# Performance work log

Hardware: AMD Instinct MI355X
Metric: run time of the kernel (lower is better)

Reference implementation:

```python
import jax, jax.numpy as jnp
import numpy as np

D_MODEL = 1024
POOL = 2048
K = 16
D_FF = 4096
N_HEADS = 16
TEMP = 1.0
EPS = 1e-5


def _ln(x, g, b):
    mu = jnp.mean(x, axis=-1, keepdims=True)
    var = jnp.mean((x - mu) ** 2, axis=-1, keepdims=True)
    return (x - mu) * jax.lax.rsqrt(var + EPS) * g + b


def setup_inputs() -> dict:
    key = jax.random.key(0)
    ks = jax.random.split(key, 12)
    s = 0.02
    return {
        "x": jax.random.normal(ks[0], (4, 1024, D_MODEL), jnp.float32),
        "w_router": s * jax.random.normal(ks[1], (D_MODEL, POOL), jnp.float32),
        "b_router": jnp.zeros((POOL,), jnp.float32),
        "firing": s * jax.random.normal(ks[2], (POOL, D_FF), jnp.float32),
        "w_pool_out": s * jax.random.normal(ks[3], (D_FF, D_MODEL), jnp.float32),
        "b_pool_out": jnp.zeros((D_MODEL,), jnp.float32),
        "w_in": s * jax.random.normal(ks[4], (D_MODEL, 3 * D_MODEL), jnp.float32),
        "b_in": jnp.zeros((3 * D_MODEL,), jnp.float32),
        "w_attn_out": s * jax.random.normal(ks[5], (D_MODEL, D_MODEL), jnp.float32),
        "b_attn_out": jnp.zeros((D_MODEL,), jnp.float32),
        "g1": jnp.ones((D_MODEL,), jnp.float32),
        "beta1": jnp.zeros((D_MODEL,), jnp.float32),
        "g2": jnp.ones((D_MODEL,), jnp.float32),
        "beta2": jnp.zeros((D_MODEL,), jnp.float32),
    }


def reference(x, w_router, b_router, firing, w_pool_out, b_pool_out,
              w_in, b_in, w_attn_out, b_attn_out, g1, beta1, g2, beta2):
    B, S, D = x.shape
    Hd = D // N_HEADS
    # --- Context router: score every neuron, select top-k, softmax weights ---
    scores = x @ w_router + b_router                      # [B,S,P]
    top_vals, top_idx = jax.lax.top_k(scores, K)          # [B,S,K]
    weights = jax.nn.softmax(top_vals / TEMP, axis=-1)    # [B,S,K]
    # --- Neuron pool: gather firing patterns, weighted combine, GELU, project ---
    patterns = firing[top_idx]                            # [B,S,K,d_ff] gather
    combined = jnp.einsum('bsk,bskf->bsf', weights, patterns)  # [B,S,d_ff]
    neuron_out = jax.nn.gelu(combined, approximate=False) @ w_pool_out + b_pool_out  # [B,S,D]
    # --- Self-attention over neuron_out (dropout inactive at eval) ---
    qkv = neuron_out @ w_in + b_in                        # [B,S,3D]
    q, k, v = jnp.split(qkv, 3, axis=-1)
    q = q.reshape(B, S, N_HEADS, Hd).transpose(0, 2, 1, 3)
    k = k.reshape(B, S, N_HEADS, Hd).transpose(0, 2, 1, 3)
    v = v.reshape(B, S, N_HEADS, Hd).transpose(0, 2, 1, 3)
    logits = jnp.einsum('bhqd,bhkd->bhqk', q, k) / jnp.sqrt(jnp.float32(Hd))
    probs = jax.nn.softmax(logits, axis=-1)
    ctx = jnp.einsum('bhqk,bhkd->bhqd', probs, v)
    ctx = ctx.transpose(0, 2, 1, 3).reshape(B, S, D)
    attn_out = ctx @ w_attn_out + b_attn_out
    # --- Residuals + norms ---
    h = _ln(x + attn_out, g1, beta1)
    out = _ln(h + neuron_out, g2, beta2)
    return out
```

## Files before the change

### kernel.cpp

```cpp
#include <hip/hip_runtime.h>
#include <math.h>

typedef __attribute__((ext_vector_type(8))) __bf16 bf16x8;
typedef __attribute__((ext_vector_type(4))) __bf16 bf16x4;
typedef __attribute__((ext_vector_type(4))) float f32x4;

#define DEV static __device__ __forceinline__

DEV float b2f(unsigned short u){ union{unsigned i; float f;} c; c.i=((unsigned)u)<<16; return c.f; }
DEV unsigned short f2b(float f){
  union{float f; unsigned u;} c; c.f=f;
  unsigned r = 0x7FFFu + ((c.u>>16)&1u);
  return (unsigned short)((c.u + r)>>16);
}
DEV unsigned pack2(float a, float b){ return (unsigned)f2b(a) | ((unsigned)f2b(b)<<16); }
DEV float gelu_exact(float x){ return 0.5f*x*(1.f+erff(x*0.70710678118654752f)); }

typedef __attribute__((address_space(1))) void gas_void;
typedef __attribute__((address_space(3))) void las_void;
DEV void gload_lds16(const unsigned short* g, unsigned short* l){
  __builtin_amdgcn_global_load_lds((const gas_void*)g, (las_void*)l, 16, 0, 0);
}

template<int N> DEV void waitcnt_vm(){
  if constexpr(N==0)      asm volatile("s_waitcnt vmcnt(0)" ::: "memory");
  else if constexpr(N==2) asm volatile("s_waitcnt vmcnt(2)" ::: "memory");
  else if constexpr(N==3) asm volatile("s_waitcnt vmcnt(3)" ::: "memory");
  else if constexpr(N==4) asm volatile("s_waitcnt vmcnt(4)" ::: "memory");
  else if constexpr(N==6) asm volatile("s_waitcnt vmcnt(6)" ::: "memory");
  else if constexpr(N==8) asm volatile("s_waitcnt vmcnt(8)" ::: "memory");
  else                    asm volatile("s_waitcnt vmcnt(0)" ::: "memory");
}

__global__ __launch_bounds__(256) void k_cast_bf16(const float* __restrict__ in,
                                                   unsigned short* __restrict__ out, long n4)
{
  long i = (long)blockIdx.x*256 + threadIdx.x;
  if (i >= n4) return;
  float4 v = ((const float4*)in)[i];
  ushort4 o; o.x=f2b(v.x); o.y=f2b(v.y); o.z=f2b(v.z); o.w=f2b(v.w);
  ((ushort4*)out)[i] = o;
}

__global__ __launch_bounds__(256) void k_transpose_cast(const float* __restrict__ in,
                                                        unsigned short* __restrict__ out,
                                                        int R, int C)
{
  __shared__ float tile[32][33];
  const int tc = blockIdx.x*32, tr = blockIdx.y*32;
  {
    const int r = threadIdx.x>>3, c4 = (threadIdx.x&7)*4;
    float4 v = *(const float4*)&in[(long)(tr+r)*C + tc+c4];
    tile[r][c4+0]=v.x; tile[r][c4+1]=v.y; tile[r][c4+2]=v.z; tile[r][c4+3]=v.w;
  }
  __syncthreads();
  {
    const int c = threadIdx.x>>3, r4 = (threadIdx.x&7)*4;
    ushort4 o;
    o.x = f2b(tile[r4+0][c]); o.y = f2b(tile[r4+1][c]);
    o.z = f2b(tile[r4+2][c]); o.w = f2b(tile[r4+3][c]);
    *(ushort4*)&out[(long)(tc+c)*R + tr+r4] = o;
  }
}

template<int WR, int WC, int FM, int FN, int OMODE>
__global__ __launch_bounds__(WR*WC*64, 2) void k_gemm_bt(
  const unsigned short* __restrict__ A, long lda, long sAb,
  const unsigned short* __restrict__ Bt, long ldb, long sBb,
  float* __restrict__ Cf, unsigned short* __restrict__ Cb, long ldc, long sCb,
  const float* __restrict__ bias, int Kiters)
{
  constexpr int WAVES = WR*WC;
  constexpr int BM = WR*FM*16, BN = WC*FN*16;
  constexpr int AR16 = BM/16, TOT16 = (BM+BN)/16;
  constexpr int UNITS = TOT16/WAVES;
  static_assert(TOT16 % WAVES == 0, "stage units must split across waves");
  __shared__ __align__(16) unsigned short S[3][TOT16*512];
  const int tid = threadIdx.x;
  const int wave = tid>>6, lane = tid&63;
  const int wr = wave/WC, wc = wave%WC;
  const int l15 = lane&15, lhi = lane>>4;
  const int lrow = lane>>2;
  const int lcol = ((lane&3) ^ ((lrow>>1)&3))*8;

  const int gx = gridDim.x;
  const int nwg = gx*gridDim.y;
  const int id = blockIdx.y*gx + blockIdx.x;
  const int sid = (id&7)*(nwg>>3) + (id>>3);
  const long bm = (long)(sid / gx)*BM, bn = (long)(sid % gx)*BN;

  const unsigned short* Ab  = A  + (long)blockIdx.z*sAb + bm*lda;
  const unsigned short* Btb = Bt + (long)blockIdx.z*sBb + bn*ldb;

  f32x4 acc[FM][FN];
  #pragma unroll
  for (int i=0;i<FM;i++)
    #pragma unroll
    for (int j=0;j<FN;j++) acc[i][j] = (f32x4){0.f,0.f,0.f,0.f};

  auto STAGE = [&](int kt, int buf){
    const long k0 = (long)kt*32;
    #pragma unroll
    for (int u=0; u<UNITS; ++u) {
      const int t = wave + u*WAVES;
      const unsigned short* g;
      if (t < AR16) g = Ab  + (long)(t*16 + lrow)*lda + k0 + lcol;
      else          g = Btb + (long)((t-AR16)*16 + lrow)*ldb + k0 + lcol;
      gload_lds16(g, &S[buf][t*512]);
    }
  };
  auto COMPUTE = [&](int buf){
    const unsigned short* Sb = S[buf];
    bf16x8 bfr[FN];
    #pragma unroll
    for (int j=0;j<FN;j++) {
      const int r = wc*(FN*16) + j*16 + l15;
      bfr[j] = *(const bf16x8*)&Sb[BM*32 + r*32 + ((lhi ^ ((r>>1)&3))*8)];
    }
    #pragma unroll
    for (int i=0;i<FM;i++) {
      const int r = wr*(FM*16) + i*16 + l15;
      bf16x8 a = *(const bf16x8*)&Sb[r*32 + ((lhi ^ ((r>>1)&3))*8)];
      #pragma unroll
      for (int j=0;j<FN;j++)
        acc[i][j] = __builtin_amdgcn_mfma_f32_16x16x32_bf16(a, bfr[j], acc[i][j], 0,0,0);
    }
  };

  STAGE(0, 0);
  if (Kiters > 1) STAGE(1, 1);
  for (int kt=0; kt<Kiters; ++kt) {
    if (kt+1 < Kiters) waitcnt_vm<UNITS>();
    else               waitcnt_vm<0>();
    __builtin_amdgcn_s_barrier();
    __builtin_amdgcn_sched_barrier(0);
    COMPUTE(kt%3);
    if (kt+2 < Kiters) STAGE(kt+2, (kt+2)%3);
  }

  #pragma unroll
  for (int i=0;i<FM;i++) {
    #pragma unroll
    for (int j=0;j<FN;j++) {
      long col = bn + wc*(FN*16) + j*16 + l15;
      float bb = bias ? bias[col] : 0.f;
      #pragma unroll
      for (int q=0;q<4;q++) {
        long row = bm + wr*(FM*16) + i*16 + lhi*4 + q;
        float v = acc[i][j][q] + bb;
        long off = (long)blockIdx.z*sCb + row*ldc + col;
        if constexpr (OMODE==0 || OMODE==2) Cf[off] = v;
        if constexpr (OMODE==1 || OMODE==2) Cb[off] = f2b(v);
      }
    }
  }
}

__global__ __launch_bounds__(256) void k_combine_bias_bf16(
    const unsigned short* __restrict__ p, long sz, const float* __restrict__ bias,
    unsigned short* __restrict__ outb)
{
  const long t = blockIdx.x;
  const int tid = threadIdx.x;
  ushort4 a = ((const ushort4*)(p + t*1024))[tid];
  ushort4 b = ((const ushort4*)(p + sz + t*1024))[tid];
  float4 bi = ((const float4*)bias)[tid];
  ushort4 o;
  o.x = f2b(b2f(a.x)+b2f(b.x)+bi.x); o.y = f2b(b2f(a.y)+b2f(b.y)+bi.y);
  o.z = f2b(b2f(a.z)+b2f(b.z)+bi.z); o.w = f2b(b2f(a.w)+b2f(b.w)+bi.w);
  ((ushort4*)(outb + t*1024))[tid] = o;
}

__global__ __launch_bounds__(256) void k_topk_softmax(const unsigned short* __restrict__ scores,
                                                      int* __restrict__ topidx,
                                                      float* __restrict__ topw)
{
  const int tid = threadIdx.x, wave = tid>>6, lane = tid&63;
  const long t = blockIdx.x;
  const unsigned short* row = scores + t*2048;
  const int base = wave*512 + lane*8;
  unsigned k0,k1,k2,k3,k4,k5,k6,k7;
  {
    uint4 v4 = *(const uint4*)(row + base);
    unsigned short u[8] = {
      (unsigned short)(v4.x&0xFFFF),(unsigned short)(v4.x>>16),
      (unsigned short)(v4.y&0xFFFF),(unsigned short)(v4.y>>16),
      (unsigned short)(v4.z&0xFFFF),(unsigned short)(v4.z>>16),
      (unsigned short)(v4.w&0xFFFF),(unsigned short)(v4.w>>16) };
    unsigned kk[8];
    #pragma unroll
    for (int e=0;e<8;e++){
      unsigned m = (u[e]&0x8000u) ? (unsigned)(~u[e] & 0xFFFFu)
                                  : ((unsigned)u[e] | 0x8000u);
      kk[e] = (m<<16) | (unsigned)(2047 - (base+e));
    }
    k0=kk[0];k1=kk[1];k2=kk[2];k3=kk[3];k4=kk[4];k5=kk[5];k6=kk[6];k7=kk[7];
  }
  #define CX(x,y) { unsigned mx = x>y?x:y, mn = x>y?y:x; x=mx; y=mn; }
  CX(k0,k1) CX(k2,k3) CX(k4,k5) CX(k6,k7)
  CX(k0,k2) CX(k1,k3) CX(k4,k6) CX(k5,k7)
  CX(k1,k2) CX(k5,k6)
  CX(k0,k4) CX(k1,k5) CX(k2,k6) CX(k3,k7)
  CX(k2,k4) CX(k3,k5)
  CX(k1,k2) CX(k3,k4) CX(k5,k6)
  #undef CX

  __shared__ unsigned wk[4][16];
  unsigned my1 = 0;
  for (int it=0; it<16; ++it){
    unsigned best = k0;
    #pragma unroll
    for (int off=1; off<64; off<<=1){
      unsigned o = __shfl_xor(best, off);
      best = o>best ? o : best;
    }
    if (lane==it) my1 = best;
    bool own = (k0==best);
    k0 = own?k1:k0; k1 = own?k2:k1; k2 = own?k3:k2; k3 = own?k4:k3;
    k4 = own?k5:k4; k5 = own?k6:k5; k6 = own?k7:k6; k7 = own?0u:k7;
  }
  if (lane < 16) wk[wave][lane] = my1;
  __syncthreads();
  if (wave == 0){
    unsigned c = wk[lane>>4][lane&15];
    unsigned my2 = 0;
    for (int it=0; it<16; ++it){
      unsigned best = c;
      #pragma unroll
      for (int off=1; off<64; off<<=1){
        unsigned o = __shfl_xor(best, off);
        best = o>best ? o : best;
      }
      if (lane==it) my2 = best;
      c = (c==best) ? 0u : c;
    }
    int idx = 2047 - (int)(my2 & 0x7FFu);
    float val = -1e30f;
    if (lane < 16) val = b2f(row[idx]);
    float m0 = __shfl(val, 0);
    float e = (lane < 16) ? __expf(val - m0) : 0.f;
    float s = e;
    #pragma unroll
    for (int off=1; off<64; off<<=1) s += __shfl_xor(s, off);
    if (lane < 16){
      topw[t*16+lane]   = e/s;
      topidx[t*16+lane] = idx;
    }
  }
}

__global__ __launch_bounds__(256) void k_gather_gelu(const int* __restrict__ topidx,
                                                     const float* __restrict__ topw,
                                                     const unsigned short* __restrict__ firing,
                                                     unsigned short* __restrict__ gact)
{
  __shared__ int idx[4][16]; __shared__ float w[4][16];
  const int tid = threadIdx.x;
  const int c = blockIdx.x & 7;
  const long t0 = (long)(blockIdx.x >> 3) * 4;
  if (tid < 64) {
    int tok = tid >> 4, k = tid & 15;
    idx[tok][k] = topidx[(t0+tok)*16 + k];
    w[tok][k]   = topw[(t0+tok)*16 + k];
  }
  __syncthreads();
  const int tok = tid >> 6, lane = tid & 63;
  const int f0 = c*512 + lane*8;
  float acc[8] = {0,0,0,0,0,0,0,0};
  #pragma unroll
  for (int k=0;k<16;k++) {
    uint4 v = *(const uint4*)(firing + (long)idx[tok][k]*4096 + f0);
    const unsigned short* pu = (const unsigned short*)&v;
    float wk = w[tok][k];
    #pragma unroll
    for (int e=0;e<8;e++) acc[e] += wk * b2f(pu[e]);
  }
  float g[8];
  #pragma unroll
  for (int e=0;e<8;e++) g[e] = gelu_exact(acc[e]);
  uint4 ov;
  ov.x = pack2(g[0],g[1]); ov.y = pack2(g[2],g[3]);
  ov.z = pack2(g[4],g[5]); ov.w = pack2(g[6],g[7]);
  *(uint4*)(gact + (t0+tok)*4096 + f0) = ov;
}

__global__ __launch_bounds__(256) void k_vtrans(const unsigned short* __restrict__ qkv,
                                                unsigned short* __restrict__ vT)
{
  __shared__ unsigned short tile[64][65];
  int bh = blockIdx.y; int b = bh>>4, h = bh&15;
  long t0 = (long)blockIdx.x*64;
  const int tid = threadIdx.x;
  #pragma unroll
  for (int s=0;s<16;s++) {
    int i = tid + s*256;
    int r = i>>6, c = i&63;
    tile[r][c] = qkv[ (long)(b*1024 + t0 + r)*3072 + 2048 + h*64 + c ];
  }
  __syncthreads();
  #pragma unroll
  for (int s=0;s<16;s++) {
    int i = tid + s*256;
    int c = i>>6, r = i&63;
    vT[ (long)bh*65536 + (long)c*1024 + t0 + r ] = tile[r][c];
  }
}

__global__ __launch_bounds__(512, 4) void k_flash_attn(
  const unsigned short* __restrict__ qkv,
  const unsigned short* __restrict__ vT,
  unsigned short* __restrict__ ctx)
{
  __shared__ __align__(16) unsigned short Ks[2][128*64];
  __shared__ __align__(16) unsigned short Vs[2][64*128];
  const int tid = threadIdx.x;
  const int wave = tid>>6, lane = tid&63;
  const int l15 = lane&15, lhi = lane>>4;
  const int bh = blockIdx.x, b = bh>>4, h = bh&15;
  const long q0 = (long)blockIdx.y*128;
  const unsigned short* Qg = qkv + ((long)b*1024 + q0)*3072 + h*64;
  const unsigned short* Kg = qkv + (long)b*1024*3072 + 1024 + h*64;
  const unsigned short* Vg = vT + (long)bh*65536;

  auto STAGE_KV = [&](int t, int s){
    const long kv0 = (long)t*128;
    const int sr = lane>>3, sc = (lane&7)^sr;
    #pragma unroll
    for (int uu=0; uu<2; ++uu){
      int u = wave + uu*8;
      gload_lds16(Kg + (kv0 + u*8 + sr)*3072 + sc*8, &Ks[s][u*512]);
    }
    const int vc = (lane&15) ^ ((wave&1)*4 + lhi);
    #pragma unroll
    for (int uu=0; uu<2; ++uu){
      int u = wave + uu*8;
      gload_lds16(Vg + (long)(u*4+lhi)*1024 + kv0 + vc*8, &Vs[s][u*512]);
    }
  };

  STAGE_KV(0, 0);

  bf16x8 qf[2];
  {
    const long r = wave*16 + l15;
    qf[0] = *(const bf16x8*)(Qg + r*3072 + lhi*8);
    qf[1] = *(const bf16x8*)(Qg + r*3072 + 32 + lhi*8);
  }
  __syncthreads();

  f32x4 acco[4];
  #pragma unroll
  for (int nf=0;nf<4;nf++) acco[nf] = (f32x4){0.f,0.f,0.f,0.f};
  float m_run = -1e30f, l_run = 0.f;

  int sel = 0;
  for (int t=0; t<8; ++t) {
    if (t < 7) STAGE_KV(t+1, sel^1);
    f32x4 accs[8];
    #pragma unroll
    for (int fk=0;fk<8;fk++){
      accs[fk] = (f32x4){0.f,0.f,0.f,0.f};
      const int r = fk*16 + l15;
      bf16x8 k0 = *(const bf16x8*)&Ks[sel][r*64 + ((lhi^(r&7))*8)];
      accs[fk] = __builtin_amdgcn_mfma_f32_16x16x32_bf16(k0, qf[0], accs[fk],0,0,0);
      bf16x8 k1 = *(const bf16x8*)&Ks[sel][r*64 + (((4+lhi)^(r&7))*8)];
      accs[fk] = __builtin_amdgcn_mfma_f32_16x16x32_bf16(k1, qf[1], accs[fk],0,0,0);
    }
    float mt = -1e30f;
    #pragma unroll
    for (int fk=0;fk<8;fk++)
      #pragma unroll
      for (int q=0;q<4;q++) mt = fmaxf(mt, accs[fk][q]);
    mt = fmaxf(mt, __shfl_xor(mt,16));
    mt = fmaxf(mt, __shfl_xor(mt,32));
    mt *= 0.125f;
    if (!__all(mt <= m_run + 8.f)) {
      float mnew = fmaxf(m_run, mt);
      float fj = __expf(m_run - mnew);
      l_run *= fj;
      #pragma unroll
      for (int q=0;q<4;q++){
        float fr = __shfl(fj, (lane&48)|(lhi*4+q));
        #pragma unroll
        for (int nf=0;nf<4;nf++) acco[nf][q] *= fr;
      }
      m_run = mnew;
    }
    bf16x8 pa[4];
    float ssum = 0.f;
    #pragma unroll
    for (int fk=0;fk<8;fk++)
      #pragma unroll
      for (int q=0;q<4;q++){
        float p = __expf(accs[fk][q]*0.125f - m_run);
        ssum += p;
        pa[fk>>1][(fk&1)*4+q] = (__bf16)p;
      }
    ssum += __shfl_xor(ssum,16);
    ssum += __shfl_xor(ssum,32);
    l_run += ssum;
    #pragma unroll
    for (int kk=0;kk<4;kk++)
      #pragma unroll
      for (int nf=0;nf<4;nf++){
        const int rv = nf*16 + l15;
        const int cb = kk*4 + (lhi>>1);
        bf16x4 v0 = *(const bf16x4*)&Vs[sel][rv*128 + (( cb   ^(l15&7))*8) + (lhi&1)*4];
        bf16x4 v1 = *(const bf16x4*)&Vs[sel][rv*128 + (((cb+2)^(l15&7))*8) + (lhi&1)*4];
        bf16x8 vb = __builtin_shufflevector(v0, v1, 0,1,2,3,4,5,6,7);
        acco[nf] = __builtin_amdgcn_mfma_f32_16x16x32_bf16(pa[kk], vb, acco[nf],0,0,0);
      }
    __syncthreads();
    sel ^= 1;
  }

  #pragma unroll
  for (int q=0;q<4;q++){
    float lr = __shfl(l_run, (lane&48)|(lhi*4+q));
    float inv = 1.f/lr;
    long row = q0 + wave*16 + lhi*4 + q;
    #pragma unroll
    for (int nf=0;nf<4;nf++)
      ctx[((long)b*1024 + row)*1024 + h*64 + nf*16 + l15] = f2b(acco[nf][q]*inv);
  }
}

__global__ __launch_bounds__(256) void k_ln2(const float* __restrict__ x,
                                             const unsigned short* __restrict__ attnb,
                                             const unsigned short* __restrict__ neub,
                                             const float* __restrict__ g1,
                                             const float* __restrict__ be1,
                                             const float* __restrict__ g2,
                                             const float* __restrict__ be2,
                                             float* __restrict__ out)
{
  const long t = blockIdx.x;
  const int tid = threadIdx.x;
  const int wave = tid>>6, lane = tid&63;
  __shared__ float s1[4], s2[4], s3[4], s4[4];
  float4 xv = ((const float4*)(x + t*1024))[tid];
  ushort4 ua = ((const ushort4*)(attnb + t*1024))[tid];
  float4 sv = { xv.x + b2f(ua.x), xv.y + b2f(ua.y),
                xv.z + b2f(ua.z), xv.w + b2f(ua.w) };
  float sum = sv.x+sv.y+sv.z+sv.w;
  float sq  = sv.x*sv.x + sv.y*sv.y + sv.z*sv.z + sv.w*sv.w;
  #pragma unroll
  for (int off=32; off; off>>=1){ sum += __shfl_xor(sum,off); sq += __shfl_xor(sq,off); }
  if (lane==0){ s1[wave]=sum; s2[wave]=sq; }
  __syncthreads();
  sum = s1[0]+s1[1]+s1[2]+s1[3];
  sq  = s2[0]+s2[1]+s2[2]+s2[3];
  float mu  = sum * (1.f/1024.f);
  float var = sq * (1.f/1024.f) - mu*mu;
  float rs  = rsqrtf(var + 1e-5f);
  float4 g1v  = ((const float4*)g1)[tid];
  float4 be1v = ((const float4*)be1)[tid];
  ushort4 un = ((const ushort4*)(neub + t*1024))[tid];
  float4 hv = { (sv.x-mu)*rs*g1v.x + be1v.x + b2f(un.x),
                (sv.y-mu)*rs*g1v.y + be1v.y + b2f(un.y),
                (sv.z-mu)*rs*g1v.z + be1v.z + b2f(un.z),
                (sv.w-mu)*rs*g1v.w + be1v.w + b2f(un.w) };
  float sum2 = hv.x+hv.y+hv.z+hv.w;
  float sq2  = hv.x*hv.x + hv.y*hv.y + hv.z*hv.z + hv.w*hv.w;
  #pragma unroll
  for (int off=32; off; off>>=1){ sum2 += __shfl_xor(sum2,off); sq2 += __shfl_xor(sq2,off); }
  if (lane==0){ s3[wave]=sum2; s4[wave]=sq2; }
  __syncthreads();
  sum2 = s3[0]+s3[1]+s3[2]+s3[3];
  sq2  = s4[0]+s4[1]+s4[2]+s4[3];
  float mu2  = sum2 * (1.f/1024.f);
  float var2 = sq2 * (1.f/1024.f) - mu2*mu2;
  float rs2  = rsqrtf(var2 + 1e-5f);
  float4 g2v  = ((const float4*)g2)[tid];
  float4 be2v = ((const float4*)be2)[tid];
  float4 ov = { (hv.x-mu2)*rs2*g2v.x + be2v.x,
                (hv.y-mu2)*rs2*g2v.y + be2v.y,
                (hv.z-mu2)*rs2*g2v.z + be2v.z,
                (hv.w-mu2)*rs2*g2v.w + be2v.w };
  ((float4*)(out + t*1024))[tid] = ov;
}

extern "C" void kernel_launch(void* const* d_in, const int* in_sizes, int n_in,
                              void* d_out, int out_size, void* d_ws, size_t ws_size,
                              hipStream_t stream)
{
  const float* x        = (const float*)d_in[0];
  const float* w_router = (const float*)d_in[1];
  const float* b_router = (const float*)d_in[2];
  const float* firing   = (const float*)d_in[3];
  const float* w_pool   = (const float*)d_in[4];
  const float* b_pool   = (const float*)d_in[5];
  const float* w_in     = (const float*)d_in[6];
  const float* b_in     = (const float*)d_in[7];
  const float* w_ao     = (const float*)d_in[8];
  const float* b_ao     = (const float*)d_in[9];
  const float* g1       = (const float*)d_in[10];
  const float* be1      = (const float*)d_in[11];
  const float* g2       = (const float*)d_in[12];
  const float* be2      = (const float*)d_in[13];
  float* out = (float*)d_out;
  char* ws = (char*)d_ws;

  unsigned short* xb    = (unsigned short*)(ws + 0);
  unsigned short* wrT   = (unsigned short*)(ws + 8388608);
  unsigned short* firb  = (unsigned short*)(ws + 12582912);
  unsigned short* wpoT  = (unsigned short*)(ws + 29360128);
  unsigned short* winT  = (unsigned short*)(ws + 37748736);
  unsigned short* waoT  = (unsigned short*)(ws + 44040192);
  unsigned short* scoresb = (unsigned short*)(ws + 46137344);
  unsigned short* gact  = (unsigned short*)(ws + 46137344);
  int*    topi          = (int*)(ws + 79691776);
  float*  topw          = (float*)(ws + 79953920);
  unsigned short* attnb = (unsigned short*)(ws + 80216064);
  unsigned short* neub  = (unsigned short*)(ws + 96993280);
  unsigned short* qkvb  = (unsigned short*)(ws + 105381888);
  unsigned short* vT    = (unsigned short*)(ws + 130547712);
  unsigned short* ctx   = (unsigned short*)(ws + 138936320);
  unsigned short* poolpb= (unsigned short*)(ws + 130547712);

  if (ws_size < 164102144u) return;

  k_cast_bf16<<<4096, 256, 0, stream>>>(x, xb, 4096L*1024/4);
  k_cast_bf16<<<8192, 256, 0, stream>>>(firing, firb, 2048L*4096/4);
  k_transpose_cast<<<dim3(2048/32, 1024/32), 256, 0, stream>>>(w_router, wrT, 1024, 2048);
  k_transpose_cast<<<dim3(1024/32, 4096/32), 256, 0, stream>>>(w_pool,   wpoT, 4096, 1024);
  k_transpose_cast<<<dim3(3072/32, 1024/32), 256, 0, stream>>>(w_in,     winT, 1024, 3072);
  k_transpose_cast<<<dim3(1024/32, 1024/32), 256, 0, stream>>>(w_ao,     waoT, 1024, 1024);

  k_gemm_bt<2,2,4,4,1><<<dim3(16,32,1),256,0,stream>>>(xb,1024,0, wrT,1024,0,
        nullptr,scoresb,2048,0, b_router, 32);
  k_topk_softmax<<<4096,256,0,stream>>>(scoresb, topi, topw);
  k_gather_gelu<<<8192,256,0,stream>>>(topi, topw, firb, gact);

  k_gemm_bt<2,2,4,4,1><<<dim3(8,32,2),256,0,stream>>>(gact,4096,2048, wpoT,4096,2048,
        nullptr,poolpb,1024,4194304, nullptr, 64);
  k_combine_bias_bf16<<<4096,256,0,stream>>>(poolpb, 4194304, b_pool, neub);

  k_gemm_bt<2,2,4,4,1><<<dim3(24,32,1),256,0,stream>>>(neub,1024,0, winT,1024,0,
        nullptr,qkvb,3072,0, b_in, 32);

  k_vtrans<<<dim3(16,64),256,0,stream>>>(qkvb, vT);
  k_flash_attn<<<dim3(64,8),512,0,stream>>>(qkvb, vT, ctx);

  k_gemm_bt<2,2,4,2,1><<<dim3(16,32,1),256,0,stream>>>(ctx,1024,0, waoT,1024,0,
        nullptr,attnb,1024,0, b_ao, 32);

  k_ln2<<<4096,256,0,stream>>>(x, attnb, neub, g1, be1, g2, be2, out);
}
```

Before: 262.0 us.

## Merge weight/input prep kernels into one launch; read K directly from global in attention

Replaces six separate cast/transpose-cast launches with a single k_prep kernel that dispatches on block index, cutting launch overhead and tail gaps between small kernels. In flash attention, K tiles are no longer staged through LDS via async global-to-LDS loads; each lane loads its K fragments straight from global memory while only V stays double-buffered in LDS. This halves attention LDS use, which may raise occupancy, but K loads become exposed global latency with strided rows rather than prefetched tiles.

```diff
diff --git a/kernel.cpp b/kernel.cpp
--- a/kernel.cpp
+++ b/kernel.cpp
@@ -32,30 +32,37 @@
   else                    asm volatile("s_waitcnt vmcnt(0)" ::: "memory");
 }
 
-__global__ __launch_bounds__(256) void k_cast_bf16(const float* __restrict__ in,
-                                                   unsigned short* __restrict__ out, long n4)
-{
-  long i = (long)blockIdx.x*256 + threadIdx.x;
-  if (i >= n4) return;
+DEV void dev_cast(const float* in, unsigned short* out, long i){
   float4 v = ((const float4*)in)[i];
   ushort4 o; o.x=f2b(v.x); o.y=f2b(v.y); o.z=f2b(v.z); o.w=f2b(v.w);
   ((ushort4*)out)[i] = o;
 }
-
-__global__ __launch_bounds__(256) void k_transpose_cast(const float* __restrict__ in,
-                                                        unsigned short* __restrict__ out,
-                                                        int R, int C)
+__global__ __launch_bounds__(256) void k_prep(
+    const float* __restrict__ x,        unsigned short* __restrict__ xb,
+    const float* __restrict__ firing,   unsigned short* __restrict__ firb,
+    const float* __restrict__ w_router, unsigned short* __restrict__ wrT,
+    const float* __restrict__ w_pool,   unsigned short* __restrict__ wpoT,
+    const float* __restrict__ w_in,     unsigned short* __restrict__ winT,
+    const float* __restrict__ w_ao,     unsigned short* __restrict__ waoT)
 {
   __shared__ float tile[32][33];
-  const int tc = blockIdx.x*32, tr = blockIdx.y*32;
+  const int id = blockIdx.x, tid = threadIdx.x;
+  if (id < 4096) { dev_cast(x, xb, (long)id*256 + tid); return; }
+  if (id < 12288) { dev_cast(firing, firb, (long)(id-4096)*256 + tid); return; }
+  const float* in; unsigned short* out; int R, C, bx, by;
+  if (id < 14336) { int i2=id-12288; in=w_router; out=wrT; R=1024; C=2048; bx=i2&63;  by=i2>>6; }
+  else if (id < 18432) { int i2=id-14336; in=w_pool; out=wpoT; R=4096; C=1024; bx=i2&31; by=i2>>5; }
+  else if (id < 21504) { int i2=id-18432; in=w_in;  out=winT; R=1024; C=3072; bx=i2%96; by=i2/96; }
+  else { int i2=id-21504; in=w_ao; out=waoT; R=1024; C=1024; bx=i2&31; by=i2>>5; }
+  const int tc = bx*32, tr = by*32;
   {
-    const int r = threadIdx.x>>3, c4 = (threadIdx.x&7)*4;
+    const int r = tid>>3, c4 = (tid&7)*4;
     float4 v = *(const float4*)&in[(long)(tr+r)*C + tc+c4];
     tile[r][c4+0]=v.x; tile[r][c4+1]=v.y; tile[r][c4+2]=v.z; tile[r][c4+3]=v.w;
   }
   __syncthreads();
   {
-    const int c = threadIdx.x>>3, r4 = (threadIdx.x&7)*4;
+    const int c = tid>>3, r4 = (tid&7)*4;
     ushort4 o;
     o.x = f2b(tile[r4+0][c]); o.y = f2b(tile[r4+1][c]);
     o.z = f2b(tile[r4+2][c]); o.w = f2b(tile[r4+3][c]);
@@ -311,7 +318,6 @@
   const unsigned short* __restrict__ vT,
   unsigned short* __restrict__ ctx)
 {
-  __shared__ __align__(16) unsigned short Ks[2][128*64];
   __shared__ __align__(16) unsigned short Vs[2][64*128];
   const int tid = threadIdx.x;
   const int wave = tid>>6, lane = tid&63;
@@ -322,14 +328,8 @@
   const unsigned short* Kg = qkv + (long)b*1024*3072 + 1024 + h*64;
   const unsigned short* Vg = vT + (long)bh*65536;
 
-  auto STAGE_KV = [&](int t, int s){
+  auto STAGE_V = [&](int t, int s){
     const long kv0 = (long)t*128;
-    const int sr = lane>>3, sc = (lane&7)^sr;
-    #pragma unroll
-    for (int uu=0; uu<2; ++uu){
-      int u = wave + uu*8;
-      gload_lds16(Kg + (kv0 + u*8 + sr)*3072 + sc*8, &Ks[s][u*512]);
-    }
     const int vc = (lane&15) ^ ((wave&1)*4 + lhi);
     #pragma unroll
     for (int uu=0; uu<2; ++uu){
@@ -338,7 +338,7 @@
     }
   };
 
-  STAGE_KV(0, 0);
+  STAGE_V(0, 0);
 
   bf16x8 qf[2];
   {
@@ -355,15 +355,16 @@
 
   int sel = 0;
   for (int t=0; t<8; ++t) {
-    if (t < 7) STAGE_KV(t+1, sel^1);
+    if (t < 7) STAGE_V(t+1, sel^1);
+    const unsigned short* Kt = Kg + (long)t*128*3072;
     f32x4 accs[8];
     #pragma unroll
     for (int fk=0;fk<8;fk++){
       accs[fk] = (f32x4){0.f,0.f,0.f,0.f};
-      const int r = fk*16 + l15;
-      bf16x8 k0 = *(const bf16x8*)&Ks[sel][r*64 + ((lhi^(r&7))*8)];
+      const unsigned short* kr = Kt + (long)(fk*16 + l15)*3072;
+      bf16x8 k0 = *(const bf16x8*)(kr + lhi*8);
       accs[fk] = __builtin_amdgcn_mfma_f32_16x16x32_bf16(k0, qf[0], accs[fk],0,0,0);
-      bf16x8 k1 = *(const bf16x8*)&Ks[sel][r*64 + (((4+lhi)^(r&7))*8)];
+      bf16x8 k1 = *(const bf16x8*)(kr + 32 + lhi*8);
       accs[fk] = __builtin_amdgcn_mfma_f32_16x16x32_bf16(k1, qf[1], accs[fk],0,0,0);
     }
     float mt = -1e30f;
@@ -520,12 +521,8 @@
 
   if (ws_size < 164102144u) return;
 
-  k_cast_bf16<<<4096, 256, 0, stream>>>(x, xb, 4096L*1024/4);
-  k_cast_bf16<<<8192, 256, 0, stream>>>(firing, firb, 2048L*4096/4);
-  k_transpose_cast<<<dim3(2048/32, 1024/32), 256, 0, stream>>>(w_router, wrT, 1024, 2048);
-  k_transpose_cast<<<dim3(1024/32, 4096/32), 256, 0, stream>>>(w_pool,   wpoT, 4096, 1024);
-  k_transpose_cast<<<dim3(3072/32, 1024/32), 256, 0, stream>>>(w_in,     winT, 1024, 3072);
-  k_transpose_cast<<<dim3(1024/32, 1024/32), 256, 0, stream>>>(w_ao,     waoT, 1024, 1024);
+  k_prep<<<22528, 256, 0, stream>>>(x, xb, firing, firb, w_router, wrT,
+                                    w_pool, wpoT, w_in, winT, w_ao, waoT);
 
   k_gemm_bt<2,2,4,4,1><<<dim3(16,32,1),256,0,stream>>>(xb,1024,0, wrT,1024,0,
         nullptr,scoresb,2048,0, b_router, 32);
```

New measurement: 292.6 us. 1.12x slower.
